# Kernel optimization log

Hardware: AMD Instinct MI355X
Metric: run time of the kernel (lower is better)

## Reference

```python
import jax, jax.numpy as jnp
import numpy as np

N, D, V, T = 2048, 64, 32000, 512
K_WTA = 256
X_DECAY, U_DECAY = 0.97, 0.97
SPIKE_RATE = 0.01
FORGET_ETA = 0.01
HOMEO_TAU = 1.0
GAMMA_MAX = 1.0


def ln_row(z, eps=1e-6):
    # torch .std is unbiased (ddof=1)
    m = z.mean(-1, keepdims=True)
    s = z.std(-1, ddof=1, keepdims=True)
    return (z - m) / (s + eps)


def setup_inputs() -> dict:
    key = jax.random.key(0)
    ks = jax.random.split(key, 6)
    return {
        "tokens": jax.random.randint(ks[0], (T,), 0, V),
        "spike_u": jax.random.uniform(ks[1], (T, N), dtype=jnp.float32),
        "E": jax.random.normal(ks[2], (D, N), dtype=jnp.float32) / np.sqrt(N).astype(np.float32),
        "Dx": jax.random.normal(ks[3], (N, D), dtype=jnp.float32) / np.sqrt(D).astype(np.float32),
        "Dy": jax.random.normal(ks[4], (N, D), dtype=jnp.float32) / np.sqrt(D).astype(np.float32),
        "token_emb": jax.random.normal(ks[5], (V, D), dtype=jnp.float32) / np.sqrt(D).astype(np.float32),
    }


def reference(tokens, spike_u, E, Dx, Dy, token_emb):
    def step(carry, inp):
        x, rho = carry
        tok, u = inp
        v_prev = token_emb[tok]                                   # (D,)
        x_t = X_DECAY * x + jax.nn.relu(Dx @ v_prev)              # (N,)
        x_t = x_t / (jnp.sum(jnp.abs(x_t)) + 1e-6)                # L1 normalize
        a_hat = ln_row(rho @ x_t)                                 # (D,) ln_before_Dy
        # branches=4 with elementwise softplus == softplus on full matvec
        y_core = jax.nn.softplus(Dy @ a_hat)                      # (N,)
        y_core = y_core + (u < SPIKE_RATE).astype(y_core.dtype)   # spike noise
        # k-WTA: keep top K_WTA entries
        _, idx = jax.lax.top_k(y_core, K_WTA)
        mask = jnp.zeros((N,), bool).at[idx].set(True)
        y_core = y_core * mask.astype(y_core.dtype)
        y_t = jax.nn.relu(y_core) * jax.nn.relu(x_t)
        # homeostasis (torch uses .item() -> constant scale)
        s = y_t.sum()
        scale = jnp.where(s > 1e-8, jnp.minimum(1.0, HOMEO_TAU / (s + 1e-8)), 1.0)
        y_t = y_t * jax.lax.stop_gradient(scale)
        v_star = ln_row(E @ y_t)                                  # (D,)
        # surprisal gain (torch uses .item() -> constant)
        p = jax.nn.softmax(v_star)
        H = -(p * jnp.log(p + 1e-12)).sum()
        gain = jnp.minimum(GAMMA_MAX, H / jnp.log(jnp.float32(D) + 1e-6) * GAMMA_MAX)
        gain = jax.lax.stop_gradient(gain)
        # dynamic top-k on x_t via rank masking (jit-safe data-dependent k)
        k_dyn = jnp.clip((N * (0.05 + 0.25 * gain)).astype(jnp.int32), 1, N)
        order = jnp.argsort(-x_t)
        ranks = jnp.zeros((N,), jnp.int32).at[order].set(jnp.arange(N, dtype=jnp.int32))
        x_t = x_t * (ranks < k_dyn).astype(x_t.dtype)
        # local forgetting on inactive columns, then Hebbian update
        inactive = (x_t <= 0).astype(rho.dtype)
        rho = rho * (1.0 - FORGET_ETA * inactive[None, :])
        rho = U_DECAY * (rho + gain * jnp.outer(v_prev, x_t))
        return (x_t, rho), v_star

    init = (jnp.zeros((N,), jnp.float32), jnp.zeros((D, N), jnp.float32))
    (_, _), v_stack = jax.lax.scan(step, init, (tokens, spike_u))
    return v_stack  # (T, D)
```

## Files before the change

### kernel.cpp

```cpp
#include <hip/hip_runtime.h>
#include <math.h>

#define NB   16
#define NTH  256
#define CH   128
#define NN   2048
#define DD   64
#define TT   512
#define KWTA 256
#define PA   65
#define PB   132

typedef float f32x4 __attribute__((ext_vector_type(4)));

struct __align__(128) BarFlag { unsigned v; unsigned pad[31]; };
__device__ BarFlag g_flag[NB];
__device__ __align__(16) float  g_rf[NB][DD];
__device__ __align__(16) double g_L1[NB];
__device__ __align__(16) float  g_xg[NN];
__device__ __align__(16) float  g_yg[NN];
__device__ __align__(16) float  g_ET[NN*DD];

__global__ void bdh_init(const float* __restrict__ E) {
  const int gid = blockIdx.x * NTH + threadIdx.x;
  if (gid < NB) g_flag[gid].v = 0u;
  for (int idx = gid; idx < NN * DD; idx += 64 * NTH) {
    const int n = idx >> 6, d = idx & 63;
    g_ET[idx] = E[(size_t)d * NN + n];
  }
}

__device__ __forceinline__ void st_coh_f32(float* p, float v) {
  asm volatile("global_store_dword %0, %1, off sc0 sc1" :: "v"(p), "v"(v) : "memory");
}
__device__ __forceinline__ void st_coh_f64(double* p, double v) {
  asm volatile("global_store_dwordx2 %0, %1, off sc0 sc1" :: "v"(p), "v"(v) : "memory");
}

__device__ __forceinline__ void bar_arrive(unsigned& epoch) {
  epoch += 1u;
  asm volatile("s_waitcnt vmcnt(0)" ::: "memory");
  __syncthreads();
  if (threadIdx.x == 0)
    __hip_atomic_store(&g_flag[blockIdx.x].v, epoch, __ATOMIC_RELAXED,
                       __HIP_MEMORY_SCOPE_AGENT);
}
__device__ __forceinline__ void bar_wait(unsigned epoch) {
  if (threadIdx.x < 64) {
    const int i = (int)threadIdx.x;
    for (;;) {
      const bool ok = (i >= NB) ||
        (__hip_atomic_load(&g_flag[i].v, __ATOMIC_RELAXED,
                           __HIP_MEMORY_SCOPE_AGENT) >= epoch);
      if (__all(ok)) break;
      __builtin_amdgcn_s_sleep(1);
    }
  }
  __syncthreads();
}

__device__ __forceinline__ double wredd(double v) {
  #pragma unroll
  for (int off = 32; off > 0; off >>= 1) v += __shfl_xor(v, off, 64);
  return v;
}
__device__ __forceinline__ float wredf(float v) {
  #pragma unroll
  for (int off = 32; off > 0; off >>= 1) v += __shfl_xor(v, off, 64);
  return v;
}

__device__ __forceinline__ unsigned select_mask(const unsigned* __restrict__ keys,
                                                int K, bool prebuilt0, int tid,
                                                unsigned* __restrict__ hist,
                                                unsigned* __restrict__ hist2,
                                                unsigned* __restrict__ cw)
{
  const int wv = tid >> 6, lane = tid & 63;
  const int sub = tid & 7;
  uint4* H4 = (uint4*)hist;
  const uint4 z4 = {0u, 0u, 0u, 0u};
  unsigned prefix = 0u, pmask = 0u;
  int remK = K;
  #pragma unroll
  for (int lev = 0; lev < 4; ++lev) {
    const int shf = 24 - 8 * lev;
    if (!(lev == 0 && prebuilt0)) {
      #pragma unroll
      for (int j = 0; j < 8; ++j)
        if ((keys[j] & pmask) == prefix)
          atomicAdd(&hist[(((keys[j] >> shf) & 255u) << 3) + sub], 1u);
    }
    __syncthreads();
    {
      const uint4 a = H4[tid * 2], bq = H4[tid * 2 + 1];
      hist2[tid] = a.x + a.y + a.z + a.w + bq.x + bq.y + bq.z + bq.w;
      H4[tid * 2] = z4;
      H4[tid * 2 + 1] = z4;
    }
    __syncthreads();
    const uint4 cc = ((const uint4*)hist2)[lane];
    unsigned c[4] = {cc.x, cc.y, cc.z, cc.w};
    unsigned s[4];
    s[3] = c[3]; s[2] = c[2] + s[3]; s[1] = c[1] + s[2]; s[0] = c[0] + s[1];
    unsigned SS = s[0];
    #pragma unroll
    for (int off = 1; off < 64; off <<= 1) {
      const unsigned o = __shfl_down(SS, off, 64);
      if (lane + off < 64) SS += o;
    }
    const unsigned T = SS - s[0];
    unsigned pk = 0u;
    #pragma unroll
    for (int k = 0; k < 4; ++k) {
      const unsigned A = s[k] + T;
      if (A >= (unsigned)remK && (A - c[k]) < (unsigned)remK)
        pk = (((unsigned)(4 * lane + k)) << 16) | (unsigned)(remK - (int)(A - c[k]));
    }
    const unsigned long long bal = __ballot(pk != 0u);
    const int src = __ffsll((long long)bal) - 1;
    pk = __shfl(pk, src, 64);
    prefix |= (pk >> 16) << shf;
    remK = (int)(pk & 0xffffu);
    pmask |= 255u << shf;
  }
  const unsigned thr = prefix;
  const unsigned R = (unsigned)remK;
  unsigned lc[8], cnt = 0u;
  #pragma unroll
  for (int j = 0; j < 8; ++j) { lc[j] = cnt; cnt += (keys[j] == thr) ? 1u : 0u; }
  unsigned e = cnt;
  #pragma unroll
  for (int off = 1; off < 64; off <<= 1) {
    const unsigned o = __shfl_up(e, off, 64);
    if (lane >= off) e += o;
  }
  if (lane == 63) cw[wv] = e;
  __syncthreads();
  unsigned base = 0u;
  for (int w = 0; w < wv; ++w) base += cw[w];
  const unsigned excl = base + e - cnt;
  unsigned mask = 0u;
  #pragma unroll
  for (int j = 0; j < 8; ++j)
    if (keys[j] > thr || (keys[j] == thr && excl + lc[j] < R)) mask |= 1u << j;
  return mask;
}

__global__ void __launch_bounds__(NTH)
bdh_main(const int* __restrict__ tokens, const float* __restrict__ spike_u,
         const float* __restrict__ Emat, const float* __restrict__ Dx,
         const float* __restrict__ Dy, const float* __restrict__ temb,
         float* __restrict__ out)
{
  __shared__ float sh_rho[DD][PB];
  __shared__ float sh_Dx[CH][PA];
  __shared__ float sh_Dy[CH][PA];
  __shared__ int   sh_tok[TT];
  __shared__ float sh_v[2][DD];
  __shared__ float sh_xstate[CH];
  __shared__ float sh_xtun[CH];
  __shared__ float sh_ahat[DD];
  __shared__ float sh_ffac[CH];
  __shared__ unsigned sh_hist[256*8];
  __shared__ unsigned sh_hist2[256];
  __shared__ unsigned sh_cw[8];
  __shared__ float sh_fmisc[4];
  __shared__ double sh_dred[8];
  __shared__ double sh_rd[4][DD];
  __shared__ float sh_gred[4][DD];
  __shared__ int   sh_aidx[KWTA];
  __shared__ float sh_aw[KWTA];

  const int tid  = threadIdx.x;
  const int b    = blockIdx.x;
  const int n0   = b * CH;
  const int i2   = tid >> 1;
  const int p2   = tid & 1;
  const int d4   = tid >> 2;
  const int p4   = tid & 3;
  const int lane = tid & 63;
  const int wv   = tid >> 6;
  const int sub  = tid & 7;
  unsigned epoch = 0u;

  for (int k = tid; k < TT; k += NTH) sh_tok[k] = tokens[k];
  for (int k = tid; k < DD*PB; k += NTH) (&sh_rho[0][0])[k] = 0.0f;
  for (int k = tid; k < 256*8; k += NTH) sh_hist[k] = 0u;
  if (tid < CH) sh_xstate[tid] = 0.0f;
  for (int r = wv; r < CH; r += 4) {
    sh_Dx[r][lane] = Dx[(size_t)(n0 + r)*DD + lane];
    sh_Dy[r][lane] = Dy[(size_t)(n0 + r)*DD + lane];
  }
  __syncthreads();
  if (tid < DD) sh_v[0][tid] = temb[(size_t)sh_tok[0]*DD + tid];
  __syncthreads();

  for (int t = 0; t < TT; ++t) {
    const int par = t & 1;

    float spu = 0.0f;
    if (p2 == 0) spu = spike_u[(size_t)t*NN + n0 + i2];
    if (t + 1 < TT && tid < DD)
      sh_v[par ^ 1][tid] = temb[(size_t)sh_tok[t + 1]*DD + tid];

    float d1 = 0.0f;
    {
      const float* dxr = &sh_Dx[i2][p2*32];
      const float* vv  = &sh_v[par][p2*32];
      #pragma unroll
      for (int j = 0; j < 32; ++j) d1 += dxr[j] * vv[j];
    }
    d1 += __shfl_xor(d1, 1, 64);
    float xnew = 0.0f;
    if (p2 == 0) {
      xnew = 0.97f * sh_xstate[i2] + fmaxf(d1, 0.0f);
      sh_xtun[i2] = xnew;
      st_coh_f32(&g_xg[n0 + i2], xnew);
    }
    {
      double v = (p2 == 0) ? (double)fabsf(xnew) : 0.0;
      v = wredd(v);
      if (lane == 0) sh_dred[wv] = v;
      __syncthreads();
      if (tid == 0) st_coh_f64(&g_L1[b],
                               sh_dred[0] + sh_dred[1] + sh_dred[2] + sh_dred[3]);
    }
    float qa = 0.0f;
    {
      const float* rr = &sh_rho[d4][0];
      #pragma unroll
      for (int j = 0; j < 32; ++j) { const int c = p4 + 4*j; qa += rr[c] * sh_xtun[c]; }
    }
    qa += __shfl_xor(qa, 1, 64);
    qa += __shfl_xor(qa, 2, 64);
    if (p4 == 0) st_coh_f32(&g_rf[b][d4], qa);
    bar_arrive(epoch);
    bar_wait(epoch);

    f32x4 xu0, xu1; float rf0, rf1, rf2, rf3; double lv;
    {
      const float*  xp = g_xg + tid*8;
      const float*  rp = &g_rf[wv*4][lane];
      const double* lp = &g_L1[lane & 15];
      asm volatile(
        "global_load_dwordx4 %0, %7, off sc0 sc1\n\t"
        "global_load_dwordx4 %1, %7, off offset:16 sc0 sc1\n\t"
        "global_load_dword %2, %8, off sc0 sc1\n\t"
        "global_load_dword %3, %8, off offset:256 sc0 sc1\n\t"
        "global_load_dword %4, %8, off offset:512 sc0 sc1\n\t"
        "global_load_dword %5, %8, off offset:768 sc0 sc1\n\t"
        "global_load_dwordx2 %6, %9, off sc0 sc1\n\t"
        "s_waitcnt vmcnt(0)"
        : "=&v"(xu0), "=&v"(xu1), "=&v"(rf0), "=&v"(rf1), "=&v"(rf2), "=&v"(rf3),
          "=&v"(lv)
        : "v"(xp), "v"(rp), "v"(lp)
        : "memory");
      __builtin_amdgcn_sched_barrier(0);
    }
    {
      double acc = 0.0;
      acc += (double)rf0; acc += (double)rf1; acc += (double)rf2; acc += (double)rf3;
      sh_rd[wv][lane] = acc;
    }
    const double L1tot = wredd((lane < 16) ? lv : 0.0);
    const float Lden = (float)L1tot + 1e-6f;
    unsigned xkeys[8];
    {
      const float xf[8] = {xu0[0],xu0[1],xu0[2],xu0[3], xu1[0],xu1[1],xu1[2],xu1[3]};
      #pragma unroll
      for (int j = 0; j < 8; ++j) xkeys[j] = __float_as_uint(xf[j] / Lden);
    }
    __syncthreads();
    if (tid < 64) {
      const double qd = sh_rd[0][tid] + sh_rd[1][tid] + sh_rd[2][tid] + sh_rd[3][tid];
      const float rf = (float)qd / Lden;
      const float mm = wredf(rf) * (1.0f/64.0f);
      const float dv = rf - mm;
      const float sd = sqrtf(wredf(dv*dv) * (1.0f/63.0f));
      sh_ahat[tid] = dv / (sd + 1e-6f);
    }
    __syncthreads();
    float d2 = 0.0f;
    {
      const float* dyr = &sh_Dy[i2][p2*32];
      const float* aa  = &sh_ahat[p2*32];
      #pragma unroll
      for (int j = 0; j < 32; ++j) d2 += dyr[j] * aa[j];
    }
    d2 += __shfl_xor(d2, 1, 64);
    if (p2 == 0) {
      const float sp = fmaxf(d2, 0.0f) + log1pf(expf(-fabsf(d2)));
      st_coh_f32(&g_yg[n0 + i2], sp + ((spu < 0.01f) ? 1.0f : 0.0f));
    }
    bar_arrive(epoch);
    bar_wait(epoch);

    unsigned ykeys[8];
    {
      f32x4 yv0, yv1;
      const float* yp = g_yg + tid*8;
      asm volatile(
        "global_load_dwordx4 %0, %2, off sc0 sc1\n\t"
        "global_load_dwordx4 %1, %2, off offset:16 sc0 sc1\n\t"
        "s_waitcnt vmcnt(0)"
        : "=&v"(yv0), "=&v"(yv1) : "v"(yp) : "memory");
      __builtin_amdgcn_sched_barrier(0);
      ykeys[0]=__float_as_uint(yv0[0]); ykeys[1]=__float_as_uint(yv0[1]);
      ykeys[2]=__float_as_uint(yv0[2]); ykeys[3]=__float_as_uint(yv0[3]);
      ykeys[4]=__float_as_uint(yv1[0]); ykeys[5]=__float_as_uint(yv1[1]);
      ykeys[6]=__float_as_uint(yv1[2]); ykeys[7]=__float_as_uint(yv1[3]);
    }
    const unsigned km = select_mask(ykeys, KWTA, false, tid,
                                    sh_hist, sh_hist2, sh_cw);
    float p[8]; unsigned nzm = 0u;
    #pragma unroll
    for (int j = 0; j < 8; ++j) {
      const float yv = __uint_as_float(ykeys[j]);
      const float xv = __uint_as_float(xkeys[j]);
      p[j] = yv * xv;
      if (((km >> j) & 1u) && xv > 0.0f) nzm |= 1u << j;
    }
    const unsigned cnt = (unsigned)__popc(nzm);
    {
      double sp = 0.0;
      #pragma unroll
      for (int j = 0; j < 8; ++j) if ((nzm >> j) & 1u) sp += (double)p[j];
      sp = wredd(sp);
      if (lane == 0) sh_dred[wv] = sp;
    }
    unsigned e = cnt;
    #pragma unroll
    for (int off = 1; off < 64; off <<= 1) {
      const unsigned o = __shfl_up(e, off, 64);
      if (lane >= off) e += o;
    }
    if (lane == 63) sh_cw[4 + wv] = e;
    __syncthreads();
    const float sf = (float)(sh_dred[0] + sh_dred[1] + sh_dred[2] + sh_dred[3]);
    const float scale = (sf > 1e-8f) ? fminf(1.0f, 1.0f/(sf + 1e-8f)) : 1.0f;
    const int m = (int)(sh_cw[4] + sh_cw[5] + sh_cw[6] + sh_cw[7]);
    {
      unsigned base = 0u;
      for (int w = 0; w < wv; ++w) base += sh_cw[4 + w];
      int pos = (int)(base + e - cnt);
      #pragma unroll
      for (int j = 0; j < 8; ++j)
        if ((nzm >> j) & 1u) { sh_aidx[pos] = 8*tid + j; sh_aw[pos] = scale * p[j]; ++pos; }
    }
    __syncthreads();
    #pragma unroll
    for (int j = 0; j < 8; ++j)
      atomicAdd(&sh_hist[(((xkeys[j] >> 24) & 255u) << 3) + sub], 1u);
    {
      float a0 = 0.0f, a1 = 0.0f, a2 = 0.0f, a3 = 0.0f;
      int i = wv;
      for (; i + 12 < m; i += 16) {
        a0 = fmaf(sh_aw[i],      g_ET[(size_t)sh_aidx[i]     *DD + lane], a0);
        a1 = fmaf(sh_aw[i + 4],  g_ET[(size_t)sh_aidx[i + 4] *DD + lane], a1);
        a2 = fmaf(sh_aw[i + 8],  g_ET[(size_t)sh_aidx[i + 8] *DD + lane], a2);
        a3 = fmaf(sh_aw[i + 12], g_ET[(size_t)sh_aidx[i + 12]*DD + lane], a3);
      }
      for (; i < m; i += 4)
        a0 = fmaf(sh_aw[i], g_ET[(size_t)sh_aidx[i]*DD + lane], a0);
      sh_gred[wv][lane] = (a0 + a1) + (a2 + a3);
    }
    __syncthreads();
    if (tid < 64) {
      const float z = sh_gred[0][tid] + sh_gred[1][tid] + sh_gred[2][tid] + sh_gred[3][tid];
      const float mn = wredf(z) * (1.0f/64.0f);
      const float dv = z - mn;
      const float sd = sqrtf(wredf(dv*dv) * (1.0f/63.0f));
      const float vs = dv / (sd + 1e-6f);
      if (b == 0) out[t*DD + tid] = vs;
      float mx = vs;
      #pragma unroll
      for (int off = 32; off > 0; off >>= 1) mx = fmaxf(mx, __shfl_xor(mx, off, 64));
      const float ex = expf(vs - mx);
      const float se = wredf(ex);
      const float pp = ex / se;
      const float ht = wredf(-pp * logf(pp + 1e-12f));
      if (tid == 0) sh_fmisc[0] = fminf(1.0f, ht / logf(64.0f));
    }
    __syncthreads();
    const float gain = sh_fmisc[0];
    int kdi = (int)(2048.0f * (0.05f + 0.25f * gain));
    kdi = kdi < 1 ? 1 : (kdi > NN ? NN : kdi);
    const unsigned xm = select_mask(xkeys, kdi, true, tid,
                                    sh_hist, sh_hist2, sh_cw);
    #pragma unroll
    for (int j = 0; j < 8; ++j) {
      const int g = 8*tid + j;
      const unsigned l = (unsigned)(g - n0);
      if (l < (unsigned)CH) {
        const float xv = __uint_as_float(xkeys[j]);
        const float v = ((xm >> j) & 1u) ? xv : 0.0f;
        sh_xstate[l] = v;
        sh_ffac[l] = (v <= 0.0f) ? (1.0f - 0.01f) : 1.0f;
      }
    }
    __syncthreads();
    {
      const float vd = sh_v[par][d4];
      float* rr = &sh_rho[d4][0];
      #pragma unroll
      for (int j = 0; j < 32; ++j) {
        const int c = p4 + 4*j;
        rr[c] = 0.97f * (rr[c]*sh_ffac[c] + gain * (vd * sh_xstate[c]));
      }
    }
    __syncthreads();
  }
}

extern "C" void kernel_launch(void* const* d_in, const int* in_sizes, int n_in,
                              void* d_out, int out_size, void* d_ws, size_t ws_size,
                              hipStream_t stream) {
  const int*   tokens = (const int*)d_in[0];
  const float* spike  = (const float*)d_in[1];
  const float* Emat   = (const float*)d_in[2];
  const float* Dx     = (const float*)d_in[3];
  const float* Dy     = (const float*)d_in[4];
  const float* temb   = (const float*)d_in[5];
  float* out = (float*)d_out;
  (void)in_sizes; (void)n_in; (void)out_size; (void)d_ws; (void)ws_size;
  bdh_init<<<dim3(64), dim3(NTH), 0, stream>>>(Emat);
  bdh_main<<<dim3(NB), dim3(NTH), 0, stream>>>(tokens, spike, Emat, Dx, Dy, temb, out);
}
```

Before: 9.701 ms.

## Prebuild first-level y histogram per block and merge via global memory

Each block builds a local histogram of the top byte of its y values before the grid barrier and publishes it to global memory. After the barrier, every block sums the 16 partial histograms instead of rebuilding the level-0 histogram over all 2048 keys. Later levels use compact 256-bin histograms without sub-bin replication, so zeroing is simpler. This trades redundant per-block level-0 atomics for 16 global loads per thread and an extra block sync before the barrier, and adds contention risk in the unreplicated shared atomics.

```diff
diff --git a/kernel.cpp b/kernel.cpp
--- a/kernel.cpp
+++ b/kernel.cpp
@@ -15,11 +15,12 @@
 
 struct __align__(128) BarFlag { unsigned v; unsigned pad[31]; };
 __device__ BarFlag g_flag[NB];
-__device__ __align__(16) float  g_rf[NB][DD];
-__device__ __align__(16) double g_L1[NB];
-__device__ __align__(16) float  g_xg[NN];
-__device__ __align__(16) float  g_yg[NN];
-__device__ __align__(16) float  g_ET[NN*DD];
+__device__ __align__(16) float    g_rf[NB][DD];
+__device__ __align__(16) double   g_L1[NB];
+__device__ __align__(16) float    g_xg[NN];
+__device__ __align__(16) float    g_yg[NN];
+__device__ __align__(16) unsigned g_yh[NB][256];
+__device__ __align__(16) float    g_ET[NN*DD];
 
 __global__ void bdh_init(const float* __restrict__ E) {
   const int gid = blockIdx.x * NTH + threadIdx.x;
@@ -31,6 +32,9 @@
 }
 
 __device__ __forceinline__ void st_coh_f32(float* p, float v) {
+  asm volatile("global_store_dword %0, %1, off sc0 sc1" :: "v"(p), "v"(v) : "memory");
+}
+__device__ __forceinline__ void st_coh_u32(unsigned* p, unsigned v) {
   asm volatile("global_store_dword %0, %1, off sc0 sc1" :: "v"(p), "v"(v) : "memory");
 }
 __device__ __forceinline__ void st_coh_f64(double* p, double v) {
@@ -70,13 +74,93 @@
   return v;
 }
 
+__device__ __forceinline__ uint2 scan256h(const unsigned* __restrict__ h, int lane,
+                                          unsigned remK) {
+  const uint4 cc = ((const uint4*)h)[lane];
+  unsigned c[4] = {cc.x, cc.y, cc.z, cc.w};
+  unsigned s[4];
+  s[3] = c[3]; s[2] = c[2] + s[3]; s[1] = c[1] + s[2]; s[0] = c[0] + s[1];
+  unsigned SS = s[0];
+  #pragma unroll
+  for (int off = 1; off < 64; off <<= 1) {
+    const unsigned o = __shfl_down(SS, off, 64);
+    if (lane + off < 64) SS += o;
+  }
+  const unsigned T = SS - s[0];
+  unsigned pk = 0u;
+  #pragma unroll
+  for (int k = 0; k < 4; ++k) {
+    const unsigned A = s[k] + T;
+    if (A >= remK && (A - c[k]) < remK)
+      pk = (((unsigned)(4 * lane + k)) << 16) | (remK - (A - c[k]));
+  }
+  const unsigned long long bal = __ballot(pk != 0u);
+  const int src = __ffsll((long long)bal) - 1;
+  pk = __shfl(pk, src, 64);
+  return make_uint2(pk >> 16, pk & 0xffffu);
+}
+
+__device__ __forceinline__ unsigned tie_mask(const unsigned* __restrict__ keys,
+                                             unsigned thr, unsigned R, int tid,
+                                             unsigned* __restrict__ cw) {
+  const int wv = tid >> 6, lane = tid & 63;
+  unsigned lc[8], cnt = 0u;
+  #pragma unroll
+  for (int j = 0; j < 8; ++j) { lc[j] = cnt; cnt += (keys[j] == thr) ? 1u : 0u; }
+  unsigned e = cnt;
+  #pragma unroll
+  for (int off = 1; off < 64; off <<= 1) {
+    const unsigned o = __shfl_up(e, off, 64);
+    if (lane >= off) e += o;
+  }
+  if (lane == 63) cw[wv] = e;
+  __syncthreads();
+  unsigned base = 0u;
+  for (int w = 0; w < wv; ++w) base += cw[w];
+  const unsigned excl = base + e - cnt;
+  unsigned mask = 0u;
+  #pragma unroll
+  for (int j = 0; j < 8; ++j)
+    if (keys[j] > thr || (keys[j] == thr && excl + lc[j] < R)) mask |= 1u << j;
+  return mask;
+}
+
+__device__ __forceinline__ unsigned select_y(const unsigned* __restrict__ keys,
+                                             int K, int tid,
+                                             const unsigned* __restrict__ h0,
+                                             unsigned* __restrict__ h1,
+                                             unsigned* __restrict__ h2,
+                                             unsigned* __restrict__ h3,
+                                             unsigned* __restrict__ cw) {
+  const int lane = tid & 63;
+  uint2 r = scan256h(h0, lane, (unsigned)K);
+  unsigned pre = r.x; unsigned remK = r.y;
+  #pragma unroll
+  for (int j = 0; j < 8; ++j)
+    if ((keys[j] >> 24) == pre) atomicAdd(&h1[(keys[j] >> 16) & 255u], 1u);
+  __syncthreads();
+  r = scan256h(h1, lane, remK); pre = (pre << 8) | r.x; remK = r.y;
+  #pragma unroll
+  for (int j = 0; j < 8; ++j)
+    if ((keys[j] >> 16) == pre) atomicAdd(&h2[(keys[j] >> 8) & 255u], 1u);
+  __syncthreads();
+  r = scan256h(h2, lane, remK); pre = (pre << 8) | r.x; remK = r.y;
+  #pragma unroll
+  for (int j = 0; j < 8; ++j)
+    if ((keys[j] >> 8) == pre) atomicAdd(&h3[keys[j] & 255u], 1u);
+  __syncthreads();
+  r = scan256h(h3, lane, remK);
+  const unsigned thr = (pre << 8) | r.x;
+  return tie_mask(keys, thr, r.y, tid, cw);
+}
+
 __device__ __forceinline__ unsigned select_mask(const unsigned* __restrict__ keys,
                                                 int K, bool prebuilt0, int tid,
                                                 unsigned* __restrict__ hist,
                                                 unsigned* __restrict__ hist2,
                                                 unsigned* __restrict__ cw)
 {
-  const int wv = tid >> 6, lane = tid & 63;
+  const int lane = tid & 63;
   const int sub = tid & 7;
   uint4* H4 = (uint4*)hist;
   const uint4 z4 = {0u, 0u, 0u, 0u};
@@ -99,52 +183,12 @@
       H4[tid * 2 + 1] = z4;
     }
     __syncthreads();
-    const uint4 cc = ((const uint4*)hist2)[lane];
-    unsigned c[4] = {cc.x, cc.y, cc.z, cc.w};
-    unsigned s[4];
-    s[3] = c[3]; s[2] = c[2] + s[3]; s[1] = c[1] + s[2]; s[0] = c[0] + s[1];
-    unsigned SS = s[0];
-    #pragma unroll
-    for (int off = 1; off < 64; off <<= 1) {
-      const unsigned o = __shfl_down(SS, off, 64);
-      if (lane + off < 64) SS += o;
-    }
-    const unsigned T = SS - s[0];
-    unsigned pk = 0u;
-    #pragma unroll
-    for (int k = 0; k < 4; ++k) {
-      const unsigned A = s[k] + T;
-      if (A >= (unsigned)remK && (A - c[k]) < (unsigned)remK)
-        pk = (((unsigned)(4 * lane + k)) << 16) | (unsigned)(remK - (int)(A - c[k]));
-    }
-    const unsigned long long bal = __ballot(pk != 0u);
-    const int src = __ffsll((long long)bal) - 1;
-    pk = __shfl(pk, src, 64);
-    prefix |= (pk >> 16) << shf;
-    remK = (int)(pk & 0xffffu);
+    const uint2 r = scan256h(hist2, lane, (unsigned)remK);
+    prefix |= r.x << shf;
+    remK = (int)r.y;
     pmask |= 255u << shf;
   }
-  const unsigned thr = prefix;
-  const unsigned R = (unsigned)remK;
-  unsigned lc[8], cnt = 0u;
-  #pragma unroll
-  for (int j = 0; j < 8; ++j) { lc[j] = cnt; cnt += (keys[j] == thr) ? 1u : 0u; }
-  unsigned e = cnt;
-  #pragma unroll
-  for (int off = 1; off < 64; off <<= 1) {
-    const unsigned o = __shfl_up(e, off, 64);
-    if (lane >= off) e += o;
-  }
-  if (lane == 63) cw[wv] = e;
-  __syncthreads();
-  unsigned base = 0u;
-  for (int w = 0; w < wv; ++w) base += cw[w];
-  const unsigned excl = base + e - cnt;
-  unsigned mask = 0u;
-  #pragma unroll
-  for (int j = 0; j < 8; ++j)
-    if (keys[j] > thr || (keys[j] == thr && excl + lc[j] < R)) mask |= 1u << j;
-  return mask;
+  return tie_mask(keys, prefix, (unsigned)remK, tid, cw);
 }
 
 __global__ void __launch_bounds__(NTH)
@@ -164,6 +208,11 @@
   __shared__ float sh_ffac[CH];
   __shared__ unsigned sh_hist[256*8];
   __shared__ unsigned sh_hist2[256];
+  __shared__ __align__(16) unsigned sh_lh[256];
+  __shared__ __align__(16) unsigned sh_h2y[256];
+  __shared__ __align__(16) unsigned sh_hl1[256];
+  __shared__ __align__(16) unsigned sh_hl2[256];
+  __shared__ __align__(16) unsigned sh_hl3[256];
   __shared__ unsigned sh_cw[8];
   __shared__ float sh_fmisc[4];
   __shared__ double sh_dred[8];
@@ -187,6 +236,7 @@
   for (int k = tid; k < TT; k += NTH) sh_tok[k] = tokens[k];
   for (int k = tid; k < DD*PB; k += NTH) (&sh_rho[0][0])[k] = 0.0f;
   for (int k = tid; k < 256*8; k += NTH) sh_hist[k] = 0u;
+  sh_lh[tid] = 0u; sh_hl1[tid] = 0u; sh_hl2[tid] = 0u; sh_hl3[tid] = 0u;
   if (tid < CH) sh_xstate[tid] = 0.0f;
   for (int r = wv; r < CH; r += 4) {
     sh_Dx[r][lane] = Dx[(size_t)(n0 + r)*DD + lane];
@@ -291,11 +341,24 @@
     d2 += __shfl_xor(d2, 1, 64);
     if (p2 == 0) {
       const float sp = fmaxf(d2, 0.0f) + log1pf(expf(-fabsf(d2)));
-      st_coh_f32(&g_yg[n0 + i2], sp + ((spu < 0.01f) ? 1.0f : 0.0f));
+      const float yv = sp + ((spu < 0.01f) ? 1.0f : 0.0f);
+      st_coh_f32(&g_yg[n0 + i2], yv);
+      atomicAdd(&sh_lh[__float_as_uint(yv) >> 24], 1u);
+    }
+    __syncthreads();
+    {
+      const unsigned c = sh_lh[tid];
+      sh_lh[tid] = 0u;
+      st_coh_u32(&g_yh[b][tid], c);
     }
     bar_arrive(epoch);
     bar_wait(epoch);
 
+    unsigned yh[NB];
+    #pragma unroll
+    for (int bb = 0; bb < NB; ++bb)
+      yh[bb] = __hip_atomic_load(&g_yh[bb][tid], __ATOMIC_RELAXED,
+                                 __HIP_MEMORY_SCOPE_AGENT);
     unsigned ykeys[8];
     {
       f32x4 yv0, yv1;
@@ -311,8 +374,16 @@
       ykeys[4]=__float_as_uint(yv1[0]); ykeys[5]=__float_as_uint(yv1[1]);
       ykeys[6]=__float_as_uint(yv1[2]); ykeys[7]=__float_as_uint(yv1[3]);
     }
-    const unsigned km = select_mask(ykeys, KWTA, false, tid,
-                                    sh_hist, sh_hist2, sh_cw);
+    {
+      unsigned hs = 0u;
+      #pragma unroll
+      for (int bb = 0; bb < NB; ++bb) hs += yh[bb];
+      sh_h2y[tid] = hs;
+    }
+    __syncthreads();
+    const unsigned km = select_y(ykeys, KWTA, tid, sh_h2y,
+                                 sh_hl1, sh_hl2, sh_hl3, sh_cw);
+    sh_hl1[tid] = 0u; sh_hl2[tid] = 0u; sh_hl3[tid] = 0u;
     float p[8]; unsigned nzm = 0u;
     #pragma unroll
     for (int j = 0; j < 8; ++j) {
```

New measurement: 9.454 ms. -2.5%, faster.
